# Optimization experiments

Measured on AMD Instinct MI355X. Metric: run time of the kernel, lower is better.

## Reference

```python
import jax, jax.numpy as jnp
import numpy as np

N, F, OUT = 8192, 256, 256


def setup_inputs() -> dict:
    key = jax.random.key(0)
    ks = jax.random.split(key, 8)
    s = 1.0 / np.sqrt(F)
    return {
        "features": jax.random.normal(ks[0], (N, F), jnp.float32),
        "key_features": jax.random.normal(ks[1], (N, F), jnp.float32),
        "adj_matrix": jax.random.uniform(ks[2], (N, N), jnp.float32),
        "W_d": jax.random.normal(ks[3], (2 * F, F), jnp.float32) * (1.0 / np.sqrt(2 * F)),
        "b_d": jnp.zeros((F,), jnp.float32),
        "W_o": jax.random.normal(ks[4], (F, OUT), jnp.float32) * s,
        "b_o": jnp.zeros((OUT,), jnp.float32),
        "W_a": jax.random.normal(ks[5], (F, F), jnp.float32) * s,
        "b_a": jnp.zeros((F,), jnp.float32),
        "W_ao": jax.random.normal(ks[6], (F, OUT), jnp.float32) * s,
        "b_ao": jnp.zeros((OUT,), jnp.float32),
    }


def reference(features, key_features, adj_matrix, W_d, b_d, W_o, b_o, W_a, b_a, W_ao, b_ao):
    n = features.shape[0]
    # masked softmax over rows; self-loop (diagonal) masked out
    neg = jnp.asarray(-1e9, adj_matrix.dtype)
    logits = adj_matrix * 5.0 + jnp.eye(n, dtype=adj_matrix.dtype) * neg
    a = jax.nn.softmax(logits, axis=-1)  # [N, N]
    # sum_j a_ij * concat(x_i, x_j) == concat(x_i * rowsum_i, (A @ X)_i)
    rowsum = jnp.sum(a, axis=-1, keepdims=True)  # == 1, kept for faithfulness
    agg = a @ features  # [N, F]
    neigh = jnp.concatenate([features * rowsum, agg], axis=-1)  # [N, 2F]
    neigh_distill = neigh @ W_d + b_d
    feature_updated = jnp.tanh((features - neigh_distill) @ W_o + b_o)
    # aggregate branch (withAgg=True)
    key_agg = (a @ key_features) @ W_a + b_a
    feature_aggregate = jnp.tanh((key_features + key_agg) @ W_ao + b_ao)
    return (feature_updated, feature_aggregate)
```

## Files before the change

### kernel.cpp

```cpp
#include <hip/hip_runtime.h>
#include <stdint.h>
#include <math.h>


typedef __attribute__((ext_vector_type(4)))  short bf16x4_t;
typedef __attribute__((ext_vector_type(8)))  short bf16x8_t;
typedef __attribute__((ext_vector_type(4)))  float f32x4_t;
typedef __attribute__((ext_vector_type(16))) float f32x16_t;

#define MFMA32(A, B, C) __builtin_amdgcn_mfma_f32_32x32x16_bf16(A, B, C, 0, 0, 0)
#define MFMA16(A, B, C) __builtin_amdgcn_mfma_f32_16x16x32_bf16(A, B, C, 0, 0, 0)

__device__ __forceinline__ unsigned short f2bf(float x) {
    union { float f; unsigned u; } c; c.f = x;
    unsigned u = c.u;
    return (unsigned short)((u + 0x7fffu + ((u >> 16) & 1u)) >> 16);
}
__device__ __forceinline__ unsigned pack2bf(float a, float b) {
    return (unsigned)f2bf(a) | ((unsigned)f2bf(b) << 16);
}
__device__ __forceinline__ float bflo(unsigned u) {
    union { unsigned u; float f; } c; c.u = u << 16; return c.f;
}
__device__ __forceinline__ float bfhi(unsigned u) {
    union { unsigned u; float f; } c; c.u = u & 0xffff0000u; return c.f;
}

__global__ __launch_bounds__(256) void transpose_blob(
    const float* __restrict__ src, unsigned short* __restrict__ Xtb, int c32base)
{
    __shared__ float tile[32][33];
    const int t = threadIdx.x;
    const int x = t & 31, y4 = (t >> 5) * 4;
    const int r0 = blockIdx.x * 32, c0 = blockIdx.y * 32;
#pragma unroll
    for (int i = 0; i < 4; ++i)
        tile[y4 + i][x] = src[(size_t)(r0 + y4 + i) * 256 + c0 + x];
    __syncthreads();
    const int s = t >> 7, lane = (t >> 1) & 63, e0 = (t & 1) * 4;
    const int kl = s * 16 + (lane >> 5) * 8 + e0;
    const int cl = lane & 31;
    unsigned short* blob = Xtb + ((size_t)blockIdx.x * 16 + (c0 >> 5) + c32base) * 1024;
    uint2 v;
    v.x = pack2bf(tile[kl][cl],     tile[kl + 1][cl]);
    v.y = pack2bf(tile[kl + 2][cl], tile[kl + 3][cl]);
    *(uint2*)(blob + t * 4) = v;
}

__global__ __launch_bounds__(256) void pack_half(
    const float* __restrict__ src, unsigned* __restrict__ dst)
{
    const int idx = blockIdx.x * 256 + threadIdx.x;
    const int row = idx >> 7, cp = idx & 127;
    float2 v = *(const float2*)(src + (size_t)row * 256 + cp * 2);
    dst[(size_t)row * 256 + cp] = pack2bf(v.x, v.y);
}

__global__ __launch_bounds__(256) void compose1(
    const float* __restrict__ W_d, const float* __restrict__ W_o,
    unsigned short* __restrict__ W1t)
{
    __shared__ float wrow[256];
    const int k = blockIdx.x, t = threadIdx.x;
    wrow[t] = W_d[(size_t)k * 256 + t];
    __syncthreads();
    float acc = 0.f;
#pragma unroll 8
    for (int m = 0; m < 256; ++m) acc = fmaf(wrow[m], W_o[(size_t)m * 256 + t], acc);
    const float v = (k < 256 ? W_o[(size_t)k * 256 + t] : 0.f) - acc;
    W1t[(size_t)t * 512 + k] = f2bf(v);
}

__global__ __launch_bounds__(256) void compose2(
    const float* __restrict__ W_a, const float* __restrict__ W_ao,
    unsigned short* __restrict__ W2t)
{
    __shared__ float wrow[256];
    const int k = blockIdx.x, t = threadIdx.x;
    float v;
    if (k < 256) {
        v = W_ao[(size_t)k * 256 + t];
    } else {
        wrow[t] = W_a[(size_t)(k - 256) * 256 + t];
        __syncthreads();
        float acc = 0.f;
#pragma unroll 8
        for (int m = 0; m < 256; ++m) acc = fmaf(wrow[m], W_ao[(size_t)m * 256 + t], acc);
        v = acc;
    }
    W2t[(size_t)t * 512 + k] = f2bf(v);
}

__global__ __launch_bounds__(256) void biasC(
    const float* __restrict__ b_d, const float* __restrict__ b_o,
    const float* __restrict__ b_a, const float* __restrict__ b_ao,
    const float* __restrict__ W_o, const float* __restrict__ W_ao,
    float* __restrict__ c1, float* __restrict__ c2)
{
    const int t = threadIdx.x;
    float a1 = 0.f, a2 = 0.f;
#pragma unroll 8
    for (int m = 0; m < 256; ++m) {
        a1 = fmaf(b_d[m], W_o [(size_t)m * 256 + t], a1);
        a2 = fmaf(b_a[m], W_ao[(size_t)m * 256 + t], a2);
    }
    c1[t] = b_o[t] - a1;
    c2[t] = b_ao[t] + a2;
}

#define ROWS 64
#define KSLICE 2048
#define NIT 64
#define NCH 16
#define ASTRIDE 36

__global__ __launch_bounds__(512, 2) void exp_gemm(
    const float* __restrict__ adj, const unsigned short* __restrict__ Xtb,
    unsigned* __restrict__ UpartB, float* __restrict__ sSp)
{
    __shared__ unsigned short sA[2][4][ROWS * ASTRIDE];

    const int t = threadIdx.x;
    const int w = t >> 6, lane = t & 63, q = lane >> 5, l31 = lane & 31;
    const int xcd = blockIdx.x & 7;
    const int h = xcd >> 1;
    const int rb = ((blockIdx.x >> 3) << 1) | (xcd & 1);
    const int row0 = rb * ROWS;
    const int kbase = h * KSLICE, jbase = h * (KSLICE / 32);

    const int srow = t >> 3, skoff = (t & 7) * 4;
    const int sgrow = row0 + srow;
    const float* adj_row = adj + (size_t)sgrow * 8192 + kbase + skoff;
    const int swoff = srow * ASTRIDE + skoff;

    const unsigned short* wb = Xtb + (size_t)(2 * w) * 1024 + lane * 8;

    float rs = 0.f;
    f32x16_t acc[2][2];
#pragma unroll
    for (int mt = 0; mt < 2; ++mt)
#pragma unroll
        for (int ct = 0; ct < 2; ++ct)
#pragma unroll
            for (int e = 0; e < 16; ++e) acc[mt][ct][e] = 0.f;

    bf16x8_t bq[2][2][4];
    float4 qaA[4], qaB[4];

    auto stageChunk = [&](int cidx, const float4 (&qa)[4], int buf) {
        unsigned short* sb = &sA[buf][0][0] + swoff;
#pragma unroll
        for (int ks = 0; ks < 4; ++ks) {
            const float4 v = qa[ks];
            float e0 = __expf(5.f * v.x);
            float e1 = __expf(5.f * v.y);
            float e2 = __expf(5.f * v.z);
            float e3 = __expf(5.f * v.w);
            const int gk = kbase + (cidx * 4 + ks) * 32 + skoff;
            if (gk + 0 == sgrow) e0 = 0.f;
            if (gk + 1 == sgrow) e1 = 0.f;
            if (gk + 2 == sgrow) e2 = 0.f;
            if (gk + 3 == sgrow) e3 = 0.f;
            rs += (e0 + e1) + (e2 + e3);
            uint2 p; p.x = pack2bf(e0, e1); p.y = pack2bf(e2, e3);
            *(uint2*)(sb + ks * (ROWS * ASTRIDE)) = p;
        }
    };

    auto phase = [&](int c, float4 (&qaPre)[4], const float4 (&qaStg)[4], int buf) {
        if (c + 2 < NCH) {
#pragma unroll
            for (int ks = 0; ks < 4; ++ks)
                qaPre[ks] = *(const float4*)(adj_row + (size_t)((c + 2) * 4 + ks) * 32);
        }
        if (c + 1 < NCH) stageChunk(c + 1, qaStg, buf ^ 1);
#pragma unroll
        for (int u = 0; u < 4; ++u) {
            const int j = c * 4 + u;
            int jn = j + 2; if (jn >= NIT) jn = 0;
            const unsigned short* bb = wb + (size_t)(jbase + jn) * 16384;
#pragma unroll
            for (int k4 = 0; k4 < 4; ++k4)
                bq[((u >> 1) ^ 1) & 1][u & 1][k4] = *(const bf16x8_t*)(bb + k4 * 512);
            const unsigned short* sa = &sA[buf][u][0] + l31 * ASTRIDE + q * 8;
            bf16x8_t af[2][2];
#pragma unroll
            for (int mt = 0; mt < 2; ++mt)
#pragma unroll
                for (int s = 0; s < 2; ++s) {
                    const unsigned short* p = sa + mt * (32 * ASTRIDE) + s * 16;
                    bf16x4_t lo = *(const bf16x4_t*)p;
                    bf16x4_t hi = *(const bf16x4_t*)(p + 4);
                    af[mt][s] = __builtin_shufflevector(lo, hi, 0, 1, 2, 3, 4, 5, 6, 7);
                }
            __builtin_amdgcn_s_setprio(1);
#pragma unroll
            for (int s = 0; s < 2; ++s)
#pragma unroll
                for (int mt = 0; mt < 2; ++mt)
#pragma unroll
                    for (int ct = 0; ct < 2; ++ct)
                        acc[mt][ct] = MFMA32(af[mt][s], bq[(u >> 1) & 1][u & 1][ct * 2 + s], acc[mt][ct]);
            __builtin_amdgcn_s_setprio(0);
        }
        asm volatile("s_waitcnt lgkmcnt(0)\n\ts_barrier" ::: "memory");
    };

#pragma unroll
    for (int ks = 0; ks < 4; ++ks)
        qaA[ks] = *(const float4*)(adj_row + (size_t)ks * 32);
#pragma unroll
    for (int ks = 0; ks < 4; ++ks)
        qaB[ks] = *(const float4*)(adj_row + (size_t)(4 + ks) * 32);
    stageChunk(0, qaA, 0);
    {
        const unsigned short* b0 = wb + (size_t)(jbase + 0) * 16384;
        const unsigned short* b1 = wb + (size_t)(jbase + 1) * 16384;
#pragma unroll
        for (int k4 = 0; k4 < 4; ++k4) {
            bq[0][0][k4] = *(const bf16x8_t*)(b0 + k4 * 512);
            bq[0][1][k4] = *(const bf16x8_t*)(b1 + k4 * 512);
        }
    }
    asm volatile("s_waitcnt lgkmcnt(0)\n\ts_barrier" ::: "memory");

    for (int c0 = 0; c0 < NCH; c0 += 2) {
        phase(c0,     qaA, qaB, 0);
        phase(c0 + 1, qaB, qaA, 1);
    }

    rs += __shfl_xor(rs, 1);
    rs += __shfl_xor(rs, 2);
    rs += __shfl_xor(rs, 4);
    if ((t & 7) == 0) sSp[h * 8192 + sgrow] = rs;

    unsigned* up = UpartB + (((size_t)h * 128 + rb) * 8 + w) * 2048 + lane;
#pragma unroll
    for (int mt = 0; mt < 2; ++mt)
#pragma unroll
        for (int ct = 0; ct < 2; ++ct)
#pragma unroll
            for (int ip = 0; ip < 8; ++ip)
                up[(size_t)(((mt * 2 + ct) * 8) + ip) * 64] =
                    pack2bf(acc[mt][ct][2 * ip], acc[mt][ct][2 * ip + 1]);
}

__global__ __launch_bounds__(256) void finalize_agg(
    const unsigned* __restrict__ UpartB, const float* __restrict__ sSp,
    unsigned* __restrict__ XcatN, unsigned* __restrict__ Kcat)
{
    __shared__ float sT[64][65];
    __shared__ float sInv[64];

    const int t = threadIdx.x;
    const int rb = blockIdx.x >> 3, wp = blockIdx.x & 7;
    const int row0 = rb * 64;

    if (t < 64) {
        const int r = row0 + t;
        sInv[t] = 1.f / (sSp[r] + sSp[8192 + r] + sSp[16384 + r] + sSp[24576 + r]);
    }

    const int i = t >> 3;
    const int l0 = (t & 7) * 8;
    const int mt = i >> 4, ct = (i >> 3) & 1, ip = i & 7;
    const int qq = l0 >> 5;
    const int rlo = mt * 32 + 2 * (ip & 1) + 8 * (ip >> 1) + 4 * qq;
    const int cbase = ct * 32 + (l0 & 31);

    float lo[8], hi[8];
#pragma unroll
    for (int j = 0; j < 8; ++j) { lo[j] = 0.f; hi[j] = 0.f; }
#pragma unroll
    for (int h = 0; h < 4; ++h) {
        const unsigned* src = UpartB + (((size_t)h * 128 + rb) * 8 + wp) * 2048
                              + (size_t)i * 64 + l0;
        const uint4 v0 = *(const uint4*)(src);
        const uint4 v1 = *(const uint4*)(src + 4);
        const unsigned vv[8] = { v0.x, v0.y, v0.z, v0.w, v1.x, v1.y, v1.z, v1.w };
#pragma unroll
        for (int j = 0; j < 8; ++j) { lo[j] += bflo(vv[j]); hi[j] += bfhi(vv[j]); }
    }
#pragma unroll
    for (int j = 0; j < 8; ++j) {
        sT[rlo][cbase + j]     = lo[j];
        sT[rlo + 1][cbase + j] = hi[j];
    }
    __syncthreads();

    const int row = t >> 2, cg = (t & 3) * 16;
    const float inv = sInv[row];
    unsigned outv[8];
#pragma unroll
    for (int j = 0; j < 8; ++j)
        outv[j] = pack2bf(sT[row][cg + 2 * j] * inv, sT[row][cg + 2 * j + 1] * inv);
    unsigned* dst = (wp < 4 ? XcatN : Kcat)
                    + (size_t)(row0 + row) * 256 + 128 + (wp & 3) * 32 + (cg >> 1);
    *(uint4*)(dst)     = *(const uint4*)(outv);
    *(uint4*)(dst + 4) = *(const uint4*)(outv + 4);
}

__global__ __launch_bounds__(256) void gemm_out(
    const unsigned short* __restrict__ Aa, const unsigned short* __restrict__ Wta,
    const float* __restrict__ ca,
    const unsigned short* __restrict__ Ab, const unsigned short* __restrict__ Wtb,
    const float* __restrict__ cb,
    float* __restrict__ outa, float* __restrict__ outb)
{
    __shared__ unsigned short sAm[32 * ASTRIDE];
    __shared__ unsigned short sB[256 * ASTRIDE];
    __shared__ float sBias[256];

    const int bid = blockIdx.x;
    const int prob = bid >> 8, tile = bid & 255;
    const unsigned short* A  = prob ? Ab  : Aa;
    const unsigned short* Wt = prob ? Wtb : Wta;
    const float* cvec        = prob ? cb  : ca;
    float* out               = prob ? outb : outa;

    const int t = threadIdx.x, w = t >> 6, lane = t & 63;
    const int m_lo = lane & 15, quad = lane >> 4;
    const int row0 = tile * 32;
    sBias[t] = cvec[t];

    f32x4_t acc[2][4];
#pragma unroll
    for (int a = 0; a < 2; ++a)
#pragma unroll
        for (int b = 0; b < 4; ++b)
#pragma unroll
            for (int e = 0; e < 4; ++e) acc[a][b][e] = 0.f;

    for (int ks = 0; ks < 16; ++ks) {
        const int k0 = ks * 32;
        __syncthreads();
        if (t < 128) {
            bf16x8_t v = *(const bf16x8_t*)(A + (size_t)(row0 + (t >> 2)) * 512 + k0 + (t & 3) * 8);
            unsigned short* d = &sAm[(t >> 2) * ASTRIDE + (t & 3) * 8];
            *(bf16x4_t*)d       = __builtin_shufflevector(v, v, 0, 1, 2, 3);
            *(bf16x4_t*)(d + 4) = __builtin_shufflevector(v, v, 4, 5, 6, 7);
        }
        {
            const unsigned short* src = Wt + (size_t)t * 512 + k0;
            unsigned short* d = &sB[t * ASTRIDE];
#pragma unroll
            for (int j = 0; j < 4; ++j) {
                bf16x8_t v = *(const bf16x8_t*)(src + j * 8);
                *(bf16x4_t*)(d + j * 8)     = __builtin_shufflevector(v, v, 0, 1, 2, 3);
                *(bf16x4_t*)(d + j * 8 + 4) = __builtin_shufflevector(v, v, 4, 5, 6, 7);
            }
        }
        __syncthreads();
        bf16x8_t a0, a1;
        {
            const unsigned short* p = &sAm[m_lo * ASTRIDE + quad * 8];
            bf16x4_t lo = *(const bf16x4_t*)p, hi = *(const bf16x4_t*)(p + 4);
            a0 = __builtin_shufflevector(lo, hi, 0, 1, 2, 3, 4, 5, 6, 7);
            p += 16 * ASTRIDE;
            lo = *(const bf16x4_t*)p; hi = *(const bf16x4_t*)(p + 4);
            a1 = __builtin_shufflevector(lo, hi, 0, 1, 2, 3, 4, 5, 6, 7);
        }
#pragma unroll
        for (int nt = 0; nt < 4; ++nt) {
            const unsigned short* p = &sB[(w * 64 + nt * 16 + m_lo) * ASTRIDE + quad * 8];
            bf16x4_t lo = *(const bf16x4_t*)p, hi = *(const bf16x4_t*)(p + 4);
            bf16x8_t b = __builtin_shufflevector(lo, hi, 0, 1, 2, 3, 4, 5, 6, 7);
            acc[0][nt] = MFMA16(a0, b, acc[0][nt]);
            acc[1][nt] = MFMA16(a1, b, acc[1][nt]);
        }
    }

#pragma unroll
    for (int mt = 0; mt < 2; ++mt)
#pragma unroll
        for (int nt = 0; nt < 4; ++nt) {
            const int col = w * 64 + nt * 16 + m_lo;
#pragma unroll
            for (int r = 0; r < 4; ++r) {
                const int row = row0 + mt * 16 + quad * 4 + r;
                out[(size_t)row * 256 + col] = tanhf(acc[mt][nt][r] + sBias[col]);
            }
        }
}

extern "C" void kernel_launch(void* const* d_in, const int* in_sizes, int n_in,
                              void* d_out, int out_size, void* d_ws, size_t ws_size,
                              hipStream_t stream) {
    const float* features = (const float*)d_in[0];
    const float* key      = (const float*)d_in[1];
    const float* adj      = (const float*)d_in[2];
    const float* W_d  = (const float*)d_in[3];
    const float* b_d  = (const float*)d_in[4];
    const float* W_o  = (const float*)d_in[5];
    const float* b_o  = (const float*)d_in[6];
    const float* W_a  = (const float*)d_in[7];
    const float* b_a  = (const float*)d_in[8];
    const float* W_ao = (const float*)d_in[9];
    const float* b_ao = (const float*)d_in[10];

    float* out1 = (float*)d_out;
    float* out2 = out1 + (size_t)8192 * 256;

    char* ws = (char*)d_ws;
    unsigned short* XcatN = (unsigned short*)(ws);
    unsigned short* Kcat  = (unsigned short*)(ws +  8388608);
    unsigned short* Xtb   = (unsigned short*)(ws + 16777216);
    unsigned*       UpartB= (unsigned*)      (ws + 25165824);
    float*          sSp   = (float*)         (ws + 58720256);
    unsigned short* W1t   = (unsigned short*)(ws + 58851328);
    unsigned short* W2t   = (unsigned short*)(ws + 59113472);
    float*          c1    = (float*)         (ws + 59375616);
    float*          c2    = (float*)         (ws + 59376640);

    dim3 blk(256);
    transpose_blob<<<dim3(256, 8), blk, 0, stream>>>(features, Xtb, 0);
    transpose_blob<<<dim3(256, 8), blk, 0, stream>>>(key, Xtb, 8);
    pack_half<<<4096, blk, 0, stream>>>(features, (unsigned*)XcatN);
    pack_half<<<4096, blk, 0, stream>>>(key, (unsigned*)Kcat);
    compose1<<<512, blk, 0, stream>>>(W_d, W_o, W1t);
    compose2<<<512, blk, 0, stream>>>(W_a, W_ao, W2t);
    biasC<<<1, blk, 0, stream>>>(b_d, b_o, b_a, b_ao, W_o, W_ao, c1, c2);

    exp_gemm<<<512, dim3(512), 0, stream>>>(adj, Xtb, UpartB, sSp);
    finalize_agg<<<1024, blk, 0, stream>>>(UpartB, sSp,
                                           (unsigned*)XcatN, (unsigned*)Kcat);

    gemm_out<<<512, blk, 0, stream>>>(XcatN, W1t, c1, Kcat, W2t, c2, out1, out2);
}
```

Baseline: 512.7 us.

## Stream exp_gemm B tiles via global_load_lds and fuse prep kernels

The main exp_gemm loop no longer loads B fragments into registers. It now issues asynchronous global-to-LDS loads (global_load_lds) into a four-slot per-wave ring buffer, with explicit vmcnt waits, and the adjacency prefetch is deepened to four smaller chunks. The aim is to free registers and hide global-load latency behind the MFMA work. Separately, pack_half is folded into transpose_blob and biasC into the compose kernels, which removes three launches. The cost is added LDS use and fragile hand-tuned vmcnt counts that can go wrong.

```diff
diff --git a/kernel.cpp b/kernel.cpp
--- a/kernel.cpp
+++ b/kernel.cpp
@@ -26,8 +26,15 @@
     union { unsigned u; float f; } c; c.u = u & 0xffff0000u; return c.f;
 }
 
+__device__ __forceinline__ void gll16(const unsigned short* g, unsigned short* l) {
+    __builtin_amdgcn_global_load_lds(
+        (const __attribute__((address_space(1))) unsigned int*)(g),
+        (__attribute__((address_space(3))) unsigned int*)(l), 16, 0, 0);
+}
+
 __global__ __launch_bounds__(256) void transpose_blob(
-    const float* __restrict__ src, unsigned short* __restrict__ Xtb, int c32base)
+    const float* __restrict__ src, unsigned short* __restrict__ Xtb,
+    unsigned* __restrict__ packdst, int c32base)
 {
     __shared__ float tile[32][33];
     const int t = threadIdx.x;
@@ -45,80 +52,67 @@
     v.x = pack2bf(tile[kl][cl],     tile[kl + 1][cl]);
     v.y = pack2bf(tile[kl + 2][cl], tile[kl + 3][cl]);
     *(uint2*)(blob + t * 4) = v;
-}
-
-__global__ __launch_bounds__(256) void pack_half(
-    const float* __restrict__ src, unsigned* __restrict__ dst)
-{
-    const int idx = blockIdx.x * 256 + threadIdx.x;
-    const int row = idx >> 7, cp = idx & 127;
-    float2 v = *(const float2*)(src + (size_t)row * 256 + cp * 2);
-    dst[(size_t)row * 256 + cp] = pack2bf(v.x, v.y);
+    const int prow = t >> 3, pc = t & 7;
+    unsigned* pd = packdst + (size_t)(r0 + prow) * 256 + (c0 >> 1) + pc * 2;
+    pd[0] = pack2bf(tile[prow][pc * 4 + 0], tile[prow][pc * 4 + 1]);
+    pd[1] = pack2bf(tile[prow][pc * 4 + 2], tile[prow][pc * 4 + 3]);
 }
 
 __global__ __launch_bounds__(256) void compose1(
     const float* __restrict__ W_d, const float* __restrict__ W_o,
-    unsigned short* __restrict__ W1t)
+    const float* __restrict__ b_d, const float* __restrict__ b_o,
+    unsigned short* __restrict__ W1t, float* __restrict__ c1)
 {
     __shared__ float wrow[256];
     const int k = blockIdx.x, t = threadIdx.x;
-    wrow[t] = W_d[(size_t)k * 256 + t];
+    const float* srcrow = (k < 512) ? (W_d + (size_t)k * 256) : b_d;
+    wrow[t] = srcrow[t];
     __syncthreads();
     float acc = 0.f;
 #pragma unroll 8
     for (int m = 0; m < 256; ++m) acc = fmaf(wrow[m], W_o[(size_t)m * 256 + t], acc);
-    const float v = (k < 256 ? W_o[(size_t)k * 256 + t] : 0.f) - acc;
-    W1t[(size_t)t * 512 + k] = f2bf(v);
+    if (k < 512)
+        W1t[(size_t)t * 512 + k] = f2bf((k < 256 ? W_o[(size_t)k * 256 + t] : 0.f) - acc);
+    else
+        c1[t] = b_o[t] - acc;
 }
 
 __global__ __launch_bounds__(256) void compose2(
     const float* __restrict__ W_a, const float* __restrict__ W_ao,
-    unsigned short* __restrict__ W2t)
+    const float* __restrict__ b_a, const float* __restrict__ b_ao,
+    unsigned short* __restrict__ W2t, float* __restrict__ c2)
 {
     __shared__ float wrow[256];
     const int k = blockIdx.x, t = threadIdx.x;
-    float v;
     if (k < 256) {
-        v = W_ao[(size_t)k * 256 + t];
-    } else {
-        wrow[t] = W_a[(size_t)(k - 256) * 256 + t];
-        __syncthreads();
-        float acc = 0.f;
+        W2t[(size_t)t * 512 + k] = f2bf(W_ao[(size_t)k * 256 + t]);
+        return;
+    }
+    const float* srcrow = (k < 512) ? (W_a + (size_t)(k - 256) * 256) : b_a;
+    wrow[t] = srcrow[t];
+    __syncthreads();
+    float acc = 0.f;
 #pragma unroll 8
-        for (int m = 0; m < 256; ++m) acc = fmaf(wrow[m], W_ao[(size_t)m * 256 + t], acc);
-        v = acc;
-    }
-    W2t[(size_t)t * 512 + k] = f2bf(v);
-}
-
-__global__ __launch_bounds__(256) void biasC(
-    const float* __restrict__ b_d, const float* __restrict__ b_o,
-    const float* __restrict__ b_a, const float* __restrict__ b_ao,
-    const float* __restrict__ W_o, const float* __restrict__ W_ao,
-    float* __restrict__ c1, float* __restrict__ c2)
-{
-    const int t = threadIdx.x;
-    float a1 = 0.f, a2 = 0.f;
-#pragma unroll 8
-    for (int m = 0; m < 256; ++m) {
-        a1 = fmaf(b_d[m], W_o [(size_t)m * 256 + t], a1);
-        a2 = fmaf(b_a[m], W_ao[(size_t)m * 256 + t], a2);
-    }
-    c1[t] = b_o[t] - a1;
-    c2[t] = b_ao[t] + a2;
+    for (int m = 0; m < 256; ++m) acc = fmaf(wrow[m], W_ao[(size_t)m * 256 + t], acc);
+    if (k < 512) W2t[(size_t)t * 512 + k] = f2bf(acc);
+    else         c2[t] = b_ao[t] + acc;
 }
 
 #define ROWS 64
 #define KSLICE 2048
 #define NIT 64
-#define NCH 16
+#define NPH 32
 #define ASTRIDE 36
+
+struct QA { float4 v[2]; };
 
 __global__ __launch_bounds__(512, 2) void exp_gemm(
     const float* __restrict__ adj, const unsigned short* __restrict__ Xtb,
     unsigned* __restrict__ UpartB, float* __restrict__ sSp)
 {
-    __shared__ unsigned short sA[2][4][ROWS * ASTRIDE];
+    __shared__ unsigned short sA[2][2][ROWS * ASTRIDE];
+    __shared__ uint4 sBq[8][4][256];
+    unsigned short* const sB = (unsigned short*)sBq;
 
     const int t = threadIdx.x;
     const int w = t >> 6, lane = t & 63, q = lane >> 5, l31 = lane & 31;
@@ -133,7 +127,8 @@
     const float* adj_row = adj + (size_t)sgrow * 8192 + kbase + skoff;
     const int swoff = srow * ASTRIDE + skoff;
 
-    const unsigned short* wb = Xtb + (size_t)(2 * w) * 1024 + lane * 8;
+    const unsigned short* XtbW = Xtb + (size_t)jbase * 16384 + (size_t)(2 * w) * 1024 + lane * 8;
+    unsigned short* const sBw = sB + (size_t)w * 4 * 2048;
 
     float rs = 0.f;
     f32x16_t acc[2][2];
@@ -144,89 +139,90 @@
 #pragma unroll
             for (int e = 0; e < 16; ++e) acc[mt][ct][e] = 0.f;
 
-    bf16x8_t bq[2][2][4];
-    float4 qaA[4], qaB[4];
-
-    auto stageChunk = [&](int cidx, const float4 (&qa)[4], int buf) {
-        unsigned short* sb = &sA[buf][0][0] + swoff;
-#pragma unroll
-        for (int ks = 0; ks < 4; ++ks) {
-            const float4 v = qa[ks];
+    QA qa0, qa1, qa2, qa3;
+
+    auto loadAdj = [&](int cidx, QA& qq) {
+        qq.v[0] = *(const float4*)(adj_row + (size_t)(cidx * 2 + 0) * 32);
+        qq.v[1] = *(const float4*)(adj_row + (size_t)(cidx * 2 + 1) * 32);
+    };
+
+    auto stageChunk = [&](int cidx, const QA& qq, int buf) {
+#pragma unroll
+        for (int ks = 0; ks < 2; ++ks) {
+            const float4 v = qq.v[ks];
             float e0 = __expf(5.f * v.x);
             float e1 = __expf(5.f * v.y);
             float e2 = __expf(5.f * v.z);
             float e3 = __expf(5.f * v.w);
-            const int gk = kbase + (cidx * 4 + ks) * 32 + skoff;
+            const int gk = kbase + (cidx * 2 + ks) * 32 + skoff;
             if (gk + 0 == sgrow) e0 = 0.f;
             if (gk + 1 == sgrow) e1 = 0.f;
             if (gk + 2 == sgrow) e2 = 0.f;
             if (gk + 3 == sgrow) e3 = 0.f;
             rs += (e0 + e1) + (e2 + e3);
             uint2 p; p.x = pack2bf(e0, e1); p.y = pack2bf(e2, e3);
-            *(uint2*)(sb + ks * (ROWS * ASTRIDE)) = p;
+            *(uint2*)(&sA[buf][ks][swoff]) = p;
         }
     };
 
-    auto phase = [&](int c, float4 (&qaPre)[4], const float4 (&qaStg)[4], int buf) {
-        if (c + 2 < NCH) {
-#pragma unroll
-            for (int ks = 0; ks < 4; ++ks)
-                qaPre[ks] = *(const float4*)(adj_row + (size_t)((c + 2) * 4 + ks) * 32);
-        }
-        if (c + 1 < NCH) stageChunk(c + 1, qaStg, buf ^ 1);
-#pragma unroll
-        for (int u = 0; u < 4; ++u) {
-            const int j = c * 4 + u;
-            int jn = j + 2; if (jn >= NIT) jn = 0;
-            const unsigned short* bb = wb + (size_t)(jbase + jn) * 16384;
-#pragma unroll
-            for (int k4 = 0; k4 < 4; ++k4)
-                bq[((u >> 1) ^ 1) & 1][u & 1][k4] = *(const bf16x8_t*)(bb + k4 * 512);
-            const unsigned short* sa = &sA[buf][u][0] + l31 * ASTRIDE + q * 8;
-            bf16x8_t af[2][2];
+    auto issueB = [&](int jn, int slot) {
+        const unsigned short* src = XtbW + (size_t)jn * 16384;
+        unsigned short* dst = sBw + slot * 2048;
+#pragma unroll
+        for (int k4 = 0; k4 < 4; ++k4)
+            gll16(src + k4 * 512, dst + k4 * 512);
+    };
+
+    auto consume = [&](int buf, int u, int slot) {
+        const unsigned short* sa = &sA[buf][u][0] + l31 * ASTRIDE + q * 8;
+        bf16x8_t af[2][2];
+#pragma unroll
+        for (int mt = 0; mt < 2; ++mt)
+#pragma unroll
+            for (int s = 0; s < 2; ++s) {
+                const unsigned short* p = sa + mt * (32 * ASTRIDE) + s * 16;
+                bf16x4_t lo = *(const bf16x4_t*)p;
+                bf16x4_t hi = *(const bf16x4_t*)(p + 4);
+                af[mt][s] = __builtin_shufflevector(lo, hi, 0, 1, 2, 3, 4, 5, 6, 7);
+            }
+        const unsigned short* sbp = sB + (size_t)(w * 4 + slot) * 2048 + lane * 8;
+        bf16x8_t bfr[4];
+#pragma unroll
+        for (int k4 = 0; k4 < 4; ++k4)
+            bfr[k4] = *(const bf16x8_t*)(sbp + k4 * 512);
+        __builtin_amdgcn_s_setprio(1);
+#pragma unroll
+        for (int s = 0; s < 2; ++s)
 #pragma unroll
             for (int mt = 0; mt < 2; ++mt)
 #pragma unroll
-                for (int s = 0; s < 2; ++s) {
-                    const unsigned short* p = sa + mt * (32 * ASTRIDE) + s * 16;
-                    bf16x4_t lo = *(const bf16x4_t*)p;
-                    bf16x4_t hi = *(const bf16x4_t*)(p + 4);
-                    af[mt][s] = __builtin_shufflevector(lo, hi, 0, 1, 2, 3, 4, 5, 6, 7);
-                }
-            __builtin_amdgcn_s_setprio(1);
-#pragma unroll
-            for (int s = 0; s < 2; ++s)
-#pragma unroll
-                for (int mt = 0; mt < 2; ++mt)
-#pragma unroll
-                    for (int ct = 0; ct < 2; ++ct)
-                        acc[mt][ct] = MFMA32(af[mt][s], bq[(u >> 1) & 1][u & 1][ct * 2 + s], acc[mt][ct]);
-            __builtin_amdgcn_s_setprio(0);
-        }
+                for (int ct = 0; ct < 2; ++ct)
+                    acc[mt][ct] = MFMA32(af[mt][s], bfr[ct * 2 + s], acc[mt][ct]);
+        __builtin_amdgcn_s_setprio(0);
+    };
+
+    auto phase = [&](int c, const QA& qstg, QA& qld, int buf) {
+        if (c + 1 < NPH) stageChunk(c + 1, qstg, buf ^ 1);
+        issueB((2 * c + 3) & 63, (2 * buf + 3) & 3);
+        asm volatile("s_waitcnt vmcnt(16)" ::: "memory");
+        consume(buf, 0, 2 * buf);
+        issueB((2 * c + 4) & 63, 2 * buf);
+        asm volatile("s_waitcnt vmcnt(14)" ::: "memory");
+        consume(buf, 1, 2 * buf + 1);
+        loadAdj((c + 4) & 31, qld);
         asm volatile("s_waitcnt lgkmcnt(0)\n\ts_barrier" ::: "memory");
     };
 
-#pragma unroll
-    for (int ks = 0; ks < 4; ++ks)
-        qaA[ks] = *(const float4*)(adj_row + (size_t)ks * 32);
-#pragma unroll
-    for (int ks = 0; ks < 4; ++ks)
-        qaB[ks] = *(const float4*)(adj_row + (size_t)(4 + ks) * 32);
-    stageChunk(0, qaA, 0);
-    {
-        const unsigned short* b0 = wb + (size_t)(jbase + 0) * 16384;
-        const unsigned short* b1 = wb + (size_t)(jbase + 1) * 16384;
-#pragma unroll
-        for (int k4 = 0; k4 < 4; ++k4) {
-            bq[0][0][k4] = *(const bf16x8_t*)(b0 + k4 * 512);
-            bq[0][1][k4] = *(const bf16x8_t*)(b1 + k4 * 512);
-        }
-    }
+    issueB(0, 0); issueB(1, 1); issueB(2, 2);
+    loadAdj(0, qa0); loadAdj(1, qa1); loadAdj(2, qa2); loadAdj(3, qa3);
+    stageChunk(0, qa0, 0);
     asm volatile("s_waitcnt lgkmcnt(0)\n\ts_barrier" ::: "memory");
 
-    for (int c0 = 0; c0 < NCH; c0 += 2) {
-        phase(c0,     qaA, qaB, 0);
-        phase(c0 + 1, qaB, qaA, 1);
+    for (int c0 = 0; c0 < NPH; c0 += 4) {
+        phase(c0 + 0, qa1, qa0, 0);
+        phase(c0 + 1, qa2, qa1, 1);
+        phase(c0 + 2, qa3, qa2, 0);
+        phase(c0 + 3, qa0, qa3, 1);
     }
 
     rs += __shfl_xor(rs, 1);
@@ -413,13 +409,10 @@
     float*          c2    = (float*)         (ws + 59376640);
 
     dim3 blk(256);
-    transpose_blob<<<dim3(256, 8), blk, 0, stream>>>(features, Xtb, 0);
-    transpose_blob<<<dim3(256, 8), blk, 0, stream>>>(key, Xtb, 8);
-    pack_half<<<4096, blk, 0, stream>>>(features, (unsigned*)XcatN);
-    pack_half<<<4096, blk, 0, stream>>>(key, (unsigned*)Kcat);
-    compose1<<<512, blk, 0, stream>>>(W_d, W_o, W1t);
-    compose2<<<512, blk, 0, stream>>>(W_a, W_ao, W2t);
-    biasC<<<1, blk, 0, stream>>>(b_d, b_o, b_a, b_ao, W_o, W_ao, c1, c2);
+    transpose_blob<<<dim3(256, 8), blk, 0, stream>>>(features, Xtb, (unsigned*)XcatN, 0);
+    transpose_blob<<<dim3(256, 8), blk, 0, stream>>>(key, Xtb, (unsigned*)Kcat, 8);
+    compose1<<<513, blk, 0, stream>>>(W_d, W_o, b_d, b_o, W1t, c1);
+    compose2<<<513, blk, 0, stream>>>(W_a, W_ao, b_a, b_ao, W2t, c2);
 
     exp_gemm<<<512, dim3(512), 0, stream>>>(adj, Xtb, UpartB, sSp);
     finalize_agg<<<1024, blk, 0, stream>>>(UpartB, sSp,
```

Result: no change. 516.4 us (+0.7%).
